# Performance work log

Hardware: AMD Instinct MI355X
Metric: run time of the kernel (lower is better)

## Reference

```python
import jax, jax.numpy as jnp
import numpy as np
import math

B, T, D = 4, 4096, 1024
N_HEAD = 16
HEAD_DIM = D // N_HEAD
BUCKET_SIZE = 64
N_HASHES = 2
N_BUCKETS = max(1, T // BUCKET_SIZE)


def rope(x):
    # x: [B, H, T, d]; faithful to the torch module (cos/sin use cat(freqs,freqs),
    # rotation interleaves even/odd pairs)
    d = x.shape[-1]
    inv_freq = 1.0 / (10000.0 ** (jnp.arange(0, d, 2, dtype=jnp.float32) / d))
    t = jnp.arange(x.shape[2], dtype=jnp.float32)
    freqs = jnp.einsum('i,j->ij', t, inv_freq)          # [T, d/2]
    emb = jnp.concatenate([freqs, freqs], axis=-1)      # [T, d]
    cos = jnp.cos(emb)[None, None, :, :]
    sin = jnp.sin(emb)[None, None, :, :]
    x1, x2 = x[..., ::2], x[..., 1::2]
    rotated = jnp.stack([-x2, x1], axis=-1).reshape(x.shape)
    return x * cos + rotated * sin


def setup_inputs() -> dict:
    key = jax.random.key(0)
    ks = jax.random.split(key, 6)
    x = jax.random.normal(ks[0], (B, T, D), dtype=jnp.float32)
    s = 1.0 / math.sqrt(D)
    W_attn = jax.random.normal(ks[1], (D, 3 * D), dtype=jnp.float32) * s
    b_attn = jnp.zeros((3 * D,), dtype=jnp.float32)
    W_proj = jax.random.normal(ks[2], (D, D), dtype=jnp.float32) * s
    b_proj = jnp.zeros((D,), dtype=jnp.float32)
    # Gaussian probe matrix (torch.manual_seed makes it a fixed constant per call)
    R = jax.random.normal(ks[3], (HEAD_DIM, N_HASHES, N_BUCKETS // 2), dtype=jnp.float32)
    return {"x": x, "W_attn": W_attn, "b_attn": b_attn,
            "W_proj": W_proj, "b_proj": b_proj, "R": R}


def reference(x, W_attn, b_attn, W_proj, b_proj, R):
    Bx, Tx, Dx = x.shape
    H, hd = N_HEAD, HEAD_DIM
    qkv = x @ W_attn + b_attn                            # [B, T, 3D]
    q, k, v = jnp.split(qkv, 3, axis=-1)

    def heads(t):
        return t.reshape(Bx, Tx, H, hd).transpose(0, 2, 1, 3)  # [B, H, T, hd]
    q, k, v = heads(q), heads(k), heads(v)
    q = rope(q)
    k = rope(k)

    qh = q.reshape(Bx * H, Tx, hd)
    kh = k.reshape(Bx * H, Tx, hd)
    vh = v.reshape(Bx * H, Tx, hd)

    # Gaussian probe hashing on queries
    proj = jnp.einsum('bnd,dhm->bnhm', qh, R)            # [BH, T, n_hashes, nb/2]
    proj = jnp.concatenate([proj, -proj], axis=-1)       # [BH, T, n_hashes, nb]
    buckets = jnp.argmax(proj, axis=-1)                  # [BH, T, n_hashes]
    b_idx = buckets[..., 0]                              # [BH, T]

    sorted_idx = jnp.argsort(b_idx, axis=-1)             # [BH, T]
    unsort_idx = jnp.argsort(sorted_idx, axis=-1)

    gidx = sorted_idx[..., None]
    q_sort = jnp.take_along_axis(qh, gidx, axis=1)
    k_sort = jnp.take_along_axis(kh, gidx, axis=1)
    v_sort = jnp.take_along_axis(vh, gidx, axis=1)

    chunk = BUCKET_SIZE * 2
    n_chunks = (Tx + chunk - 1) // chunk
    pad_len = n_chunks * chunk - Tx
    if pad_len > 0:
        pad = ((0, 0), (0, pad_len), (0, 0))
        q_sort = jnp.pad(q_sort, pad)
        k_sort = jnp.pad(k_sort, pad)
        v_sort = jnp.pad(v_sort, pad)

    qc = q_sort.reshape(Bx * H, n_chunks, chunk, hd)
    kc = k_sort.reshape(Bx * H, n_chunks, chunk, hd)
    vc = v_sort.reshape(Bx * H, n_chunks, chunk, hd)

    attn = jnp.einsum('bcid,bcjd->bcij', qc, kc) / math.sqrt(hd)
    attn = jax.nn.softmax(attn, axis=-1)
    out_local = jnp.einsum('bcij,bcjd->bcid', attn, vc)

    out_local = out_local.reshape(Bx * H, n_chunks * chunk, hd)[:, :Tx, :]
    out = jnp.take_along_axis(out_local, unsort_idx[..., None], axis=1)
    out = out.reshape(Bx, H, Tx, hd).transpose(0, 2, 1, 3).reshape(Bx, Tx, Dx)
    return out @ W_proj + b_proj
```

## Files before the change

kernel.cpp:

```cpp
#include <hip/hip_runtime.h>
#include <math.h>

#define Bz 4
#define Tz 4096
#define Dz 1024
#define Hz 16
#define HDz 64
#define BHz 64
#define Mz 16384

typedef __attribute__((ext_vector_type(8))) short short8;
typedef __attribute__((ext_vector_type(8))) __bf16 bf16x8;
typedef __attribute__((ext_vector_type(4))) float floatx4;

__device__ inline unsigned short f2bf(float f) {
    unsigned u = __float_as_uint(f);
    u = (u + 0x7fffu + ((u >> 16) & 1u)) >> 16;
    return (unsigned short)u;
}
__device__ inline float bf2f(unsigned short h) {
    return __uint_as_float(((unsigned)h) << 16);
}

__device__ __forceinline__ void g2l16(const void* g, void* l) {
    __builtin_amdgcn_global_load_lds(
        (const __attribute__((address_space(1))) unsigned int*)g,
        (__attribute__((address_space(3))) unsigned int*)l,
        16, 0, 0);
}

__global__ __launch_bounds__(256) void k_trig(float* __restrict__ tbl) {
    int t = blockIdx.x * 256 + threadIdx.x;
    float ft = (float)t;
    for (int j = 0; j < 64; ++j) {
        int kidx = (j < 32) ? j : (j - 32);
        double e = (double)(2 * kidx) / 64.0;
        float p = (float)pow(10000.0, e);
        float invf = 1.0f / p;
        float arg = ft * invf;
        tbl[t * 128 + j * 2 + 0] = cosf(arg);
        tbl[t * 128 + j * 2 + 1] = sinf(arg);
    }
}

__global__ __launch_bounds__(256) void k_cvtA(const float* __restrict__ x,
                                              unsigned short* __restrict__ xh,
                                              unsigned short* __restrict__ xl,
                                              unsigned short* __restrict__ xll)
{
    size_t i4 = (size_t)blockIdx.x * 256 + threadIdx.x;
    float4 v = *(const float4*)(x + i4 * 4);
    ushort4 h, l, l2;
    float r;
    h.x = f2bf(v.x); r = v.x - bf2f(h.x); l.x = f2bf(r); l2.x = f2bf(r - bf2f(l.x));
    h.y = f2bf(v.y); r = v.y - bf2f(h.y); l.y = f2bf(r); l2.y = f2bf(r - bf2f(l.y));
    h.z = f2bf(v.z); r = v.z - bf2f(h.z); l.z = f2bf(r); l2.z = f2bf(r - bf2f(l.z));
    h.w = f2bf(v.w); r = v.w - bf2f(h.w); l.w = f2bf(r); l2.w = f2bf(r - bf2f(l.w));
    *(ushort4*)(xh  + i4 * 4) = h;
    *(ushort4*)(xl  + i4 * 4) = l;
    *(ushort4*)(xll + i4 * 4) = l2;
}

__global__ __launch_bounds__(256) void k_cvtB(const float* __restrict__ W,
                                              unsigned short* __restrict__ wh,
                                              unsigned short* __restrict__ wl)
{
    __shared__ float tile[64][65];
    const int n0 = blockIdx.x * 64;
    const int k0 = blockIdx.y * 64;
    const int tid = threadIdx.x;
#pragma unroll
    for (int i = 0; i < 16; ++i) {
        int flat = i * 256 + tid;
        int kr = flat >> 6, nc = flat & 63;
        tile[kr][nc] = W[(size_t)(k0 + kr) * 3072 + 1024 + n0 + nc];
    }
    __syncthreads();
#pragma unroll
    for (int i = 0; i < 16; ++i) {
        int flat = i * 256 + tid;
        int nr = flat >> 6, kc = flat & 63;
        float v = tile[kc][nr];
        unsigned short h = f2bf(v);
        wh[(size_t)(n0 + nr) * 1024 + k0 + kc] = h;
        wl[(size_t)(n0 + nr) * 1024 + k0 + kc] = f2bf(v - bf2f(h));
    }
}

__global__ __launch_bounds__(256) void k_cvtBQ(const float* __restrict__ W,
                                               unsigned short* __restrict__ wh,
                                               unsigned short* __restrict__ wl,
                                               unsigned short* __restrict__ wll)
{
    __shared__ float tile[64][65];
    const int n0 = blockIdx.x * 64;
    const int k0 = blockIdx.y * 64;
    const int tid = threadIdx.x;
#pragma unroll
    for (int i = 0; i < 16; ++i) {
        int flat = i * 256 + tid;
        int kr = flat >> 6, nc = flat & 63;
        tile[kr][nc] = W[(size_t)(k0 + kr) * 3072 + n0 + nc];
    }
    __syncthreads();
#pragma unroll
    for (int i = 0; i < 16; ++i) {
        int flat = i * 256 + tid;
        int nr = flat >> 6, kc = flat & 63;
        float v = tile[kc][nr];
        unsigned short h = f2bf(v);
        float r1 = v - bf2f(h);
        unsigned short l = f2bf(r1);
        wh [(size_t)(n0 + nr) * 1024 + k0 + kc] = h;
        wl [(size_t)(n0 + nr) * 1024 + k0 + kc] = l;
        wll[(size_t)(n0 + nr) * 1024 + k0 + kc] = f2bf(r1 - bf2f(l));
    }
}

__global__ __launch_bounds__(256) void k_cvtP(const float* __restrict__ W,
                                              unsigned short* __restrict__ wh,
                                              unsigned short* __restrict__ wl)
{
    __shared__ float tile[64][65];
    const int n0 = blockIdx.x * 64;
    const int k0 = blockIdx.y * 64;
    const int tid = threadIdx.x;
#pragma unroll
    for (int i = 0; i < 16; ++i) {
        int flat = i * 256 + tid;
        int kr = flat >> 6, nc = flat & 63;
        tile[kr][nc] = W[(size_t)(k0 + kr) * 1024 + n0 + nc];
    }
    __syncthreads();
#pragma unroll
    for (int i = 0; i < 16; ++i) {
        int flat = i * 256 + tid;
        int nr = flat >> 6, kc = flat & 63;
        float v = tile[kc][nr];
        unsigned short h = f2bf(v);
        wh[(size_t)(n0 + nr) * 1024 + k0 + kc] = h;
        wl[(size_t)(n0 + nr) * 1024 + k0 + kc] = f2bf(v - bf2f(h));
    }
}

__global__ __launch_bounds__(256) void k_q6(const unsigned short* __restrict__ xh,
                                            const unsigned short* __restrict__ xl,
                                            const unsigned short* __restrict__ xll,
                                            const unsigned short* __restrict__ wh,
                                            const unsigned short* __restrict__ wl,
                                            const unsigned short* __restrict__ wll,
                                            const float* __restrict__ bias,
                                            const float* __restrict__ tbl,
                                            float* __restrict__ Qb)
{
    __shared__ unsigned short Ah[128 * 32], Al[128 * 32], A2[128 * 32];
    __shared__ unsigned short Bh[128 * 32], Bl[128 * 32], B2[128 * 32];
    const int tid = threadIdx.x;
    const int lane = tid & 63, wv = tid >> 6;
    const int hw = blockIdx.y * 8 + blockIdx.x;
    const int lg = (hw & 7) * 128 + (hw >> 3);
    const int n0 = (lg & 7) * 128;
    const int m0 = (lg >> 3) * 128;
    const int wm = (wv & 1) * 64, wn = (wv >> 1) * 64;
    const int sr = tid >> 2, sc = tid & 3;
    const int fr = lane & 15, fq = lane >> 4;

    floatx4 acc[4][4];
#pragma unroll
    for (int i = 0; i < 4; ++i)
#pragma unroll
        for (int j = 0; j < 4; ++j) acc[i][j] = (floatx4){0.f, 0.f, 0.f, 0.f};

    for (int kt = 0; kt < 1024; kt += 32) {
        __syncthreads();
#pragma unroll
        for (int s = 0; s < 2; ++s) {
            int row = s * 64 + sr;
            size_t ga = (size_t)(m0 + row) * 1024 + kt + sc * 8;
            size_t gb = (size_t)(n0 + row) * 1024 + kt + sc * 8;
            int lo = row * 32 + sc * 8;
            g2l16(xh  + ga, &Ah[lo]);
            g2l16(xl  + ga, &Al[lo]);
            g2l16(xll + ga, &A2[lo]);
            g2l16(wh  + gb, &Bh[lo]);
            g2l16(wl  + gb, &Bl[lo]);
            g2l16(wll + gb, &B2[lo]);
        }
        __syncthreads();

        bf16x8 a0[4], a1[4], a2[4];
#pragma unroll
        for (int i = 0; i < 4; ++i) {
            a0[i] = __builtin_bit_cast(bf16x8, *(const short8*)(&Ah[(wm + i * 16 + fr) * 32 + fq * 8]));
            a1[i] = __builtin_bit_cast(bf16x8, *(const short8*)(&Al[(wm + i * 16 + fr) * 32 + fq * 8]));
            a2[i] = __builtin_bit_cast(bf16x8, *(const short8*)(&A2[(wm + i * 16 + fr) * 32 + fq * 8]));
        }
#pragma unroll
        for (int j = 0; j < 4; ++j) {
            bf16x8 b0 = __builtin_bit_cast(bf16x8, *(const short8*)(&Bh[(wn + j * 16 + fr) * 32 + fq * 8]));
            bf16x8 b1 = __builtin_bit_cast(bf16x8, *(const short8*)(&Bl[(wn + j * 16 + fr) * 32 + fq * 8]));
            bf16x8 b2 = __builtin_bit_cast(bf16x8, *(const short8*)(&B2[(wn + j * 16 + fr) * 32 + fq * 8]));
#pragma unroll
            for (int i = 0; i < 4; ++i) {
                acc[i][j] = __builtin_amdgcn_mfma_f32_16x16x32_bf16(a0[i], b0, acc[i][j], 0, 0, 0);
                acc[i][j] = __builtin_amdgcn_mfma_f32_16x16x32_bf16(a0[i], b1, acc[i][j], 0, 0, 0);
                acc[i][j] = __builtin_amdgcn_mfma_f32_16x16x32_bf16(a1[i], b0, acc[i][j], 0, 0, 0);
                acc[i][j] = __builtin_amdgcn_mfma_f32_16x16x32_bf16(a1[i], b1, acc[i][j], 0, 0, 0);
                acc[i][j] = __builtin_amdgcn_mfma_f32_16x16x32_bf16(a0[i], b2, acc[i][j], 0, 0, 0);
                acc[i][j] = __builtin_amdgcn_mfma_f32_16x16x32_bf16(a2[i], b0, acc[i][j], 0, 0, 0);
            }
        }
    }

#pragma unroll
    for (int j = 0; j < 4; ++j) {
        int nn = n0 + wn + j * 16 + fr;
        float bv = bias[nn];
        int h = nn >> 6, d = nn & 63;
#pragma unroll
        for (int i = 0; i < 4; ++i) {
#pragma unroll
            for (int r = 0; r < 4; ++r) {
                int mm = m0 + wm + i * 16 + fq * 4 + r;
                int t = mm & 4095, bb = mm >> 12;
                float y = acc[i][j][r] + bv;
                float part = __shfl_xor(y, 1);
                float c = tbl[t * 128 + d * 2];
                float s = tbl[t * 128 + d * 2 + 1];
                float o = (d & 1) ? fmaf(part, s, y * c) : fmaf(-part, s, y * c);
                Qb[((size_t)(bb * 16 + h) * 4096 + t) * 64 + d] = o;
            }
        }
    }
}

__global__ __launch_bounds__(256) void k_kv(const unsigned short* __restrict__ xh,
                                            const unsigned short* __restrict__ xl,
                                            const unsigned short* __restrict__ wh,
                                            const unsigned short* __restrict__ wl,
                                            const float* __restrict__ bias,
                                            const float* __restrict__ tbl,
                                            float* __restrict__ Kb,
                                            float* __restrict__ Vb)
{
    __shared__ unsigned short Ah[128 * 32], Al[128 * 32], Bh[128 * 32], Bl[128 * 32];
    const int tid = threadIdx.x;
    const int lane = tid & 63, wv = tid >> 6;
    const int hw = blockIdx.y * 16 + blockIdx.x;
    const int lg = (hw & 7) * 256 + (hw >> 3);
    const int n0 = (lg & 15) * 128;
    const int m0 = (lg >> 4) * 128;
    const int wm = (wv & 1) * 64, wn = (wv >> 1) * 64;
    const int sr = tid >> 2, sc = tid & 3;
    const int fr = lane & 15, fq = lane >> 4;

    floatx4 acc[4][4];
#pragma unroll
    for (int i = 0; i < 4; ++i)
#pragma unroll
        for (int j = 0; j < 4; ++j) acc[i][j] = (floatx4){0.f, 0.f, 0.f, 0.f};

    for (int kt = 0; kt < 1024; kt += 32) {
        __syncthreads();
#pragma unroll
        for (int s = 0; s < 2; ++s) {
            int row = s * 64 + sr;
            size_t ga = (size_t)(m0 + row) * 1024 + kt + sc * 8;
            size_t gb = (size_t)(n0 + row) * 1024 + kt + sc * 8;
            int lo = row * 32 + sc * 8;
            g2l16(xh + ga, &Ah[lo]);
            g2l16(xl + ga, &Al[lo]);
            g2l16(wh + gb, &Bh[lo]);
            g2l16(wl + gb, &Bl[lo]);
        }
        __syncthreads();

        bf16x8 afh[4], afl[4], bfh[4], bfl[4];
#pragma unroll
        for (int i = 0; i < 4; ++i) {
            afh[i] = __builtin_bit_cast(bf16x8, *(const short8*)(&Ah[(wm + i * 16 + fr) * 32 + fq * 8]));
            afl[i] = __builtin_bit_cast(bf16x8, *(const short8*)(&Al[(wm + i * 16 + fr) * 32 + fq * 8]));
            bfh[i] = __builtin_bit_cast(bf16x8, *(const short8*)(&Bh[(wn + i * 16 + fr) * 32 + fq * 8]));
            bfl[i] = __builtin_bit_cast(bf16x8, *(const short8*)(&Bl[(wn + i * 16 + fr) * 32 + fq * 8]));
        }
#pragma unroll
        for (int i = 0; i < 4; ++i)
#pragma unroll
            for (int j = 0; j < 4; ++j) {
                acc[i][j] = __builtin_amdgcn_mfma_f32_16x16x32_bf16(afh[i], bfh[j], acc[i][j], 0, 0, 0);
                acc[i][j] = __builtin_amdgcn_mfma_f32_16x16x32_bf16(afh[i], bfl[j], acc[i][j], 0, 0, 0);
                acc[i][j] = __builtin_amdgcn_mfma_f32_16x16x32_bf16(afl[i], bfh[j], acc[i][j], 0, 0, 0);
            }
    }

#pragma unroll
    for (int j = 0; j < 4; ++j) {
        int nn = n0 + wn + j * 16 + fr;
        float bv = bias[1024 + nn];
#pragma unroll
        for (int i = 0; i < 4; ++i) {
#pragma unroll
            for (int r = 0; r < 4; ++r) {
                int mm = m0 + wm + i * 16 + fq * 4 + r;
                int t = mm & 4095, bb = mm >> 12;
                float y = acc[i][j][r] + bv;
                if (nn < 1024) {
                    int h = nn >> 6, d = nn & 63;
                    float part = __shfl_xor(y, 1);
                    float c = tbl[t * 128 + d * 2];
                    float s = tbl[t * 128 + d * 2 + 1];
                    float o = (d & 1) ? fmaf(part, s, y * c) : fmaf(-part, s, y * c);
                    Kb[((size_t)(bb * 16 + h) * 4096 + t) * 64 + d] = o;
                } else {
                    int nv = nn - 1024;
                    int h = nv >> 6, d = nv & 63;
                    Vb[((size_t)(bb * 16 + h) * 4096 + t) * 64 + d] = y;
                }
            }
        }
    }
}

__global__ __launch_bounds__(64) void k_bucket(const float* __restrict__ Q,
                                               const float* __restrict__ R,
                                               int* __restrict__ bidx)
{
    __shared__ float Qs[64][65];
    __shared__ float Rs[64][32];
    const int tid = threadIdx.x;
    const int g0 = blockIdx.x * 64;
    const int bh = g0 >> 12;
    const int t0 = g0 & 4095;
#pragma unroll
    for (int m = 0; m < 32; ++m) Rs[tid][m] = R[tid * 64 + m];
    const float* qbase = Q + ((size_t)bh * Tz + t0) * 64;
    for (int r = 0; r < 64; ++r) Qs[r][tid] = qbase[(size_t)r * 64 + tid];
    __syncthreads();

    float s[32];
#pragma unroll
    for (int m = 0; m < 32; ++m) s[m] = 0.f;
    for (int d = 0; d < 64; ++d) {
        float qd = Qs[tid][d];
#pragma unroll
        for (int m4 = 0; m4 < 8; ++m4) {
            float4 r4 = *(const float4*)(&Rs[d][m4 * 4]);
            s[m4 * 4 + 0] = fmaf(qd, r4.x, s[m4 * 4 + 0]);
            s[m4 * 4 + 1] = fmaf(qd, r4.y, s[m4 * 4 + 1]);
            s[m4 * 4 + 2] = fmaf(qd, r4.z, s[m4 * 4 + 2]);
            s[m4 * 4 + 3] = fmaf(qd, r4.w, s[m4 * 4 + 3]);
        }
    }
    float best = s[0];
    int bi = 0;
#pragma unroll
    for (int m = 1; m < 64; ++m) {
        float v = (m < 32) ? s[m] : -s[m - 32];
        if (v > best) { best = v; bi = m; }
    }
    bidx[g0 + tid] = bi;
}

__global__ __launch_bounds__(64) void k_sort(const int* __restrict__ bidx,
                                             int* __restrict__ sidx)
{
    __shared__ int lb[4096];
    __shared__ int ls[4096];
    __shared__ int runTot[64];
    __shared__ int base[64];
    const int lane = threadIdx.x;
    const int bh = blockIdx.x;
    const int* brow = bidx + (size_t)bh * 4096;
    for (int i = lane; i < 4096; i += 64) lb[i] = brow[i];
    runTot[lane] = 0;

    const unsigned long long lmask = (1ull << lane) - 1ull;
    for (int r = 0; r < 64; ++r) {
        int i = r * 64 + lane;
        int k = lb[i];
        unsigned long long m = ~0ull;
#pragma unroll
        for (int b = 0; b < 6; ++b) {
            unsigned long long bb = __ballot((k >> b) & 1);
            m &= ((k >> b) & 1) ? bb : ~bb;
        }
        int rank = __popcll(m & lmask);
        int before = runTot[k];
        lb[i] = (k << 16) | (before + rank);
        if (rank == 0) runTot[k] = before + __popcll(m);
    }
    int tot = runTot[lane];
    int run = tot;
#pragma unroll
    for (int off = 1; off < 64; off <<= 1) {
        int n = __shfl_up(run, off, 64);
        if (lane >= off) run += n;
    }
    base[lane] = run - tot;
    for (int r = 0; r < 64; ++r) {
        int i = r * 64 + lane;
        int v = lb[i];
        ls[base[v >> 16] + (v & 0xffff)] = i;
    }
    int* srow = sidx + (size_t)bh * 4096;
    for (int i = lane; i < 4096; i += 64) srow[i] = ls[i];
}

__global__ __launch_bounds__(256) void k_attn(const float* __restrict__ Q,
                                              const float* __restrict__ Kg,
                                              const float* __restrict__ Vg,
                                              const int* __restrict__ sidx,
                                              unsigned short* __restrict__ AOh,
                                              unsigned short* __restrict__ AOl)
{
    __shared__ unsigned short smem[27648];
    unsigned short* KhS = smem;
    unsigned short* KlS = smem + 9216;
    unsigned short* PbS = smem;
    unsigned short* VtS = smem + 18432;

    const int hw = blockIdx.y * 32 + blockIdx.x;
    const int lg = (hw & 7) * 256 + (hw >> 3);
    const int ch = lg & 31;
    const int bh = lg >> 5;
    const int tid = threadIdx.x;
    const int lane = tid & 63;
    const int w = tid >> 6;
    const int c = lane & 15;
    const int q = lane >> 4;
    const int* srow = sidx + (size_t)bh * Tz + ch * 128;

    {
        const int r = tid >> 1;
        const int d0 = (tid & 1) * 32;
        int orig = srow[r];
        const float* kp = Kg + ((size_t)bh * Tz + orig) * 64 + d0;
        const float* vp = Vg + ((size_t)bh * Tz + orig) * 64 + d0;
#pragma unroll
        for (int j4 = 0; j4 < 8; ++j4) {
            float4 k4 = *(const float4*)(kp + j4 * 4);
            ushort4 h4, l4;
            h4.x = f2bf(k4.x); l4.x = f2bf(k4.x - bf2f(h4.x));
            h4.y = f2bf(k4.y); l4.y = f2bf(k4.y - bf2f(h4.y));
            h4.z = f2bf(k4.z); l4.z = f2bf(k4.z - bf2f(h4.z));
            h4.w = f2bf(k4.w); l4.w = f2bf(k4.w - bf2f(h4.w));
            *(ushort4*)(&KhS[r * 72 + d0 + j4 * 4]) = h4;
            *(ushort4*)(&KlS[r * 72 + d0 + j4 * 4]) = l4;
            float4 v4 = *(const float4*)(vp + j4 * 4);
            int db = d0 + j4 * 4;
            VtS[(db + 0) * 144 + r] = f2bf(v4.x);
            VtS[(db + 1) * 144 + r] = f2bf(v4.y);
            VtS[(db + 2) * 144 + r] = f2bf(v4.z);
            VtS[(db + 3) * 144 + r] = f2bf(v4.w);
        }
    }

    bf16x8 qh[2][2], ql[2][2];
#pragma unroll
    for (int i = 0; i < 2; ++i) {
        int row = w * 32 + i * 16 + c;
        int orig = srow[row];
        const float* qp = Q + ((size_t)bh * Tz + orig) * 64 + q * 8;
#pragma unroll
        for (int kc = 0; kc < 2; ++kc) {
            float4 fa = *(const float4*)(qp + kc * 32);
            float4 fb = *(const float4*)(qp + kc * 32 + 4);
            float f[8] = {fa.x, fa.y, fa.z, fa.w, fb.x, fb.y, fb.z, fb.w};
            short8 hh, ll;
#pragma unroll
            for (int e = 0; e < 8; ++e) {
                unsigned short h = f2bf(f[e]);
                hh[e] = (short)h;
                ll[e] = (short)f2bf(f[e] - bf2f(h));
            }
            qh[i][kc] = __builtin_bit_cast(bf16x8, hh);
            ql[i][kc] = __builtin_bit_cast(bf16x8, ll);
        }
    }
    __syncthreads();

    floatx4 accs[2][8];
#pragma unroll
    for (int i = 0; i < 2; ++i)
#pragma unroll
        for (int j = 0; j < 8; ++j) accs[i][j] = (floatx4){0.f, 0.f, 0.f, 0.f};

#pragma unroll
    for (int j = 0; j < 8; ++j) {
        int n = j * 16 + c;
        bf16x8 kbh[2], kbl[2];
#pragma unroll
        for (int kc = 0; kc < 2; ++kc) {
            kbh[kc] = __builtin_bit_cast(bf16x8, *(const short8*)(&KhS[n * 72 + kc * 32 + q * 8]));
            kbl[kc] = __builtin_bit_cast(bf16x8, *(const short8*)(&KlS[n * 72 + kc * 32 + q * 8]));
        }
#pragma unroll
        for (int i = 0; i < 2; ++i)
#pragma unroll
            for (int kc = 0; kc < 2; ++kc) {
                accs[i][j] = __builtin_amdgcn_mfma_f32_16x16x32_bf16(qh[i][kc], kbh[kc], accs[i][j], 0, 0, 0);
                accs[i][j] = __builtin_amdgcn_mfma_f32_16x16x32_bf16(qh[i][kc], kbl[kc], accs[i][j], 0, 0, 0);
                accs[i][j] = __builtin_amdgcn_mfma_f32_16x16x32_bf16(ql[i][kc], kbh[kc], accs[i][j], 0, 0, 0);
            }
    }

    float linv[2][4];
#pragma unroll
    for (int i = 0; i < 2; ++i) {
#pragma unroll
        for (int r = 0; r < 4; ++r) {
            float mm = -1e30f;
#pragma unroll
            for (int j = 0; j < 8; ++j) {
                float v = accs[i][j][r] * 0.125f;
                accs[i][j][r] = v;
                mm = fmaxf(mm, v);
            }
#pragma unroll
            for (int off = 1; off < 16; off <<= 1) mm = fmaxf(mm, __shfl_xor(mm, off));
            float ss = 0.f;
#pragma unroll
            for (int j = 0; j < 8; ++j) {
                float p = expf(accs[i][j][r] - mm);
                accs[i][j][r] = p;
                ss += p;
            }
#pragma unroll
            for (int off = 1; off < 16; off <<= 1) ss += __shfl_xor(ss, off);
            linv[i][r] = 1.0f / ss;
        }
    }
    __syncthreads();

#pragma unroll
    for (int i = 0; i < 2; ++i)
#pragma unroll
        for (int j = 0; j < 8; ++j)
#pragma unroll
            for (int r = 0; r < 4; ++r)
                PbS[(w * 32 + i * 16 + q * 4 + r) * 144 + j * 16 + c] = f2bf(accs[i][j][r]);

    floatx4 acco[2][4];
#pragma unroll
    for (int i = 0; i < 2; ++i)
#pragma unroll
        for (int jf = 0; jf < 4; ++jf) acco[i][jf] = (floatx4){0.f, 0.f, 0.f, 0.f};

#pragma unroll
    for (int kc = 0; kc < 4; ++kc) {
        bf16x8 pa[2];
#pragma unroll
        for (int i = 0; i < 2; ++i)
            pa[i] = __builtin_bit_cast(bf16x8, *(const short8*)(&PbS[(w * 32 + i * 16 + c) * 144 + kc * 32 + q * 8]));
#pragma unroll
        for (int jf = 0; jf < 4; ++jf) {
            bf16x8 vb = __builtin_bit_cast(bf16x8, *(const short8*)(&VtS[(jf * 16 + c) * 144 + kc * 32 + q * 8]));
            acco[0][jf] = __builtin_amdgcn_mfma_f32_16x16x32_bf16(pa[0], vb, acco[0][jf], 0, 0, 0);
            acco[1][jf] = __builtin_amdgcn_mfma_f32_16x16x32_bf16(pa[1], vb, acco[1][jf], 0, 0, 0);
        }
    }

    const int bb = bh >> 4, hh = bh & 15;
#pragma unroll
    for (int i = 0; i < 2; ++i) {
#pragma unroll
        for (int r = 0; r < 4; ++r) {
            int row = w * 32 + i * 16 + q * 4 + r;
            int orig = srow[row];
            float inv = linv[i][r];
            size_t base = ((size_t)bb * 4096 + orig) * 1024 + hh * 64 + c;
#pragma unroll
            for (int jf = 0; jf < 4; ++jf) {
                float val = acco[i][jf][r] * inv;
                unsigned short h = f2bf(val);
                unsigned short l = f2bf(val - bf2f(h));
                AOh[base + jf * 16] = h;
                AOl[base + jf * 16] = l;
            }
        }
    }
}

__global__ __launch_bounds__(256) void k_proj(const unsigned short* __restrict__ ah,
                                              const unsigned short* __restrict__ al,
                                              const unsigned short* __restrict__ wh,
                                              const unsigned short* __restrict__ wl,
                                              const float* __restrict__ bias,
                                              float* __restrict__ Cout)
{
    __shared__ unsigned short Ah[128 * 32], Al[128 * 32], Bh[128 * 32], Bl[128 * 32];
    const int tid = threadIdx.x;
    const int lane = tid & 63, wv = tid >> 6;
    const int hw = blockIdx.y * 8 + blockIdx.x;
    const int lg = (hw & 7) * 128 + (hw >> 3);
    const int n0 = (lg & 7) * 128;
    const int m0 = (lg >> 3) * 128;
    const int wm = (wv & 1) * 64, wn = (wv >> 1) * 64;
    const int sr = tid >> 2, sc = tid & 3;
    const int fr = lane & 15, fq = lane >> 4;

    floatx4 acc[4][4];
#pragma unroll
    for (int i = 0; i < 4; ++i)
#pragma unroll
        for (int j = 0; j < 4; ++j) acc[i][j] = (floatx4){0.f, 0.f, 0.f, 0.f};

    for (int kt = 0; kt < 1024; kt += 32) {
        __syncthreads();
#pragma unroll
        for (int s = 0; s < 2; ++s) {
            int row = s * 64 + sr;
            size_t ga = (size_t)(m0 + row) * 1024 + kt + sc * 8;
            size_t gb = (size_t)(n0 + row) * 1024 + kt + sc * 8;
            int lo = row * 32 + sc * 8;
            g2l16(ah + ga, &Ah[lo]);
            g2l16(al + ga, &Al[lo]);
            g2l16(wh + gb, &Bh[lo]);
            g2l16(wl + gb, &Bl[lo]);
        }
        __syncthreads();

        bf16x8 afh[4], afl[4], bfh[4], bfl[4];
#pragma unroll
        for (int i = 0; i < 4; ++i) {
            afh[i] = __builtin_bit_cast(bf16x8, *(const short8*)(&Ah[(wm + i * 16 + fr) * 32 + fq * 8]));
            afl[i] = __builtin_bit_cast(bf16x8, *(const short8*)(&Al[(wm + i * 16 + fr) * 32 + fq * 8]));
            bfh[i] = __builtin_bit_cast(bf16x8, *(const short8*)(&Bh[(wn + i * 16 + fr) * 32 + fq * 8]));
            bfl[i] = __builtin_bit_cast(bf16x8, *(const short8*)(&Bl[(wn + i * 16 + fr) * 32 + fq * 8]));
        }
#pragma unroll
        for (int i = 0; i < 4; ++i)
#pragma unroll
            for (int j = 0; j < 4; ++j) {
                acc[i][j] = __builtin_amdgcn_mfma_f32_16x16x32_bf16(afh[i], bfh[j], acc[i][j], 0, 0, 0);
                acc[i][j] = __builtin_amdgcn_mfma_f32_16x16x32_bf16(afh[i], bfl[j], acc[i][j], 0, 0, 0);
                acc[i][j] = __builtin_amdgcn_mfma_f32_16x16x32_bf16(afl[i], bfh[j], acc[i][j], 0, 0, 0);
            }
    }

#pragma unroll
    for (int j = 0; j < 4; ++j) {
        int nn = n0 + wn + j * 16 + fr;
        float bv = bias[nn];
#pragma unroll
        for (int i = 0; i < 4; ++i) {
#pragma unroll
            for (int r = 0; r < 4; ++r) {
                int mm = m0 + wm + i * 16 + fq * 4 + r;
                Cout[(size_t)mm * 1024 + nn] = acc[i][j][r] + bv;
            }
        }
    }
}

extern "C" void kernel_launch(void* const* d_in, const int* in_sizes, int n_in,
                              void* d_out, int out_size, void* d_ws, size_t ws_size,
                              hipStream_t stream)
{
    const float* x      = (const float*)d_in[0];
    const float* W_attn = (const float*)d_in[1];
    const float* b_attn = (const float*)d_in[2];
    const float* W_proj = (const float*)d_in[3];
    const float* b_proj = (const float*)d_in[4];
    const float* R      = (const float*)d_in[5];
    float* out = (float*)d_out;

    char* ws = (char*)d_ws;
    const size_t MB = 1024 * 1024;
    float*          tbl  = (float*)(ws);
    float*          Qb   = (float*)(ws + 2 * MB);
    float*          Kb   = (float*)(ws + 66 * MB);
    unsigned short* xll  = (unsigned short*)(ws + 66 * MB);
    unsigned short* wqh  = (unsigned short*)(ws + 98 * MB);
    unsigned short* wql  = (unsigned short*)(ws + 100 * MB);
    unsigned short* wqll = (unsigned short*)(ws + 102 * MB);
    unsigned short* xh   = (unsigned short*)(ws + 130 * MB);
    unsigned short* xl   = (unsigned short*)(ws + 162 * MB);
    unsigned short* AOh  = (unsigned short*)(ws + 130 * MB);
    unsigned short* AOl  = (unsigned short*)(ws + 162 * MB);
    int*            bidx = (int*)(ws + 194 * MB);
    int*            sidx = (int*)(ws + 195 * MB);
    unsigned short* wth  = (unsigned short*)(ws + 196 * MB);
    unsigned short* wtl  = (unsigned short*)(ws + 200 * MB);
    unsigned short* wph  = (unsigned short*)(ws + 196 * MB);
    unsigned short* wpl  = (unsigned short*)(ws + 200 * MB);
    float*          Vb   = (float*)d_out;

    k_trig  <<<dim3(16),       dim3(256), 0, stream>>>(tbl);
    k_cvtA  <<<dim3(16384),    dim3(256), 0, stream>>>(x, xh, xl, xll);
    k_cvtB  <<<dim3(32, 16),   dim3(256), 0, stream>>>(W_attn, wth, wtl);
    k_cvtBQ <<<dim3(16, 16),   dim3(256), 0, stream>>>(W_attn, wqh, wql, wqll);
    k_q6    <<<dim3(8, 128),   dim3(256), 0, stream>>>(xh, xl, xll, wqh, wql, wqll, b_attn, tbl, Qb);
    k_kv    <<<dim3(16, 128),  dim3(256), 0, stream>>>(xh, xl, wth, wtl, b_attn, tbl, Kb, Vb);
    k_cvtP  <<<dim3(16, 16),   dim3(256), 0, stream>>>(W_proj, wph, wpl);
    k_bucket<<<dim3(4096),     dim3(64),  0, stream>>>(Qb, R, bidx);
    k_sort  <<<dim3(64),       dim3(64),  0, stream>>>(bidx, sidx);
    k_attn  <<<dim3(32, 64),   dim3(256), 0, stream>>>(Qb, Kb, Vb, sidx, AOh, AOl);
    k_proj  <<<dim3(8, 128),   dim3(256), 0, stream>>>(AOh, AOl, wph, wpl, b_proj, out);
}
```

Before: 824.3 us.

## Use 256x128 tiles with 512-thread blocks in GEMMs, split Q GEMM into two passes, parallelize trig table

The three split-bf16 GEMM kernels (Q, KV, proj) move from 128x128 tiles with 256 threads to 256x128 tiles with 512 threads. This raises reuse of each staged B tile and halves B traffic per output. The Q kernel now runs two K passes with only two LDS planes instead of six, trading extra A/B staging traffic for lower LDS footprint and register pressure. The trig table kernel assigns one thread per (t, j) pair instead of looping over 64 j values, so it launches far more blocks. Risks are lower occupancy from the larger blocks and the extra global reloads in the Q pass split.

Result: slower. 962.6 us (+16.8%).

```diff
diff --git a/kernel.cpp b/kernel.cpp
--- a/kernel.cpp
+++ b/kernel.cpp
@@ -30,17 +30,16 @@
 }
 
 __global__ __launch_bounds__(256) void k_trig(float* __restrict__ tbl) {
-    int t = blockIdx.x * 256 + threadIdx.x;
-    float ft = (float)t;
-    for (int j = 0; j < 64; ++j) {
-        int kidx = (j < 32) ? j : (j - 32);
-        double e = (double)(2 * kidx) / 64.0;
-        float p = (float)pow(10000.0, e);
-        float invf = 1.0f / p;
-        float arg = ft * invf;
-        tbl[t * 128 + j * 2 + 0] = cosf(arg);
-        tbl[t * 128 + j * 2 + 1] = sinf(arg);
-    }
+    int gid = blockIdx.x * 256 + threadIdx.x;
+    int t = gid >> 6;
+    int j = gid & 63;
+    int kidx = (j < 32) ? j : (j - 32);
+    double e = (double)(2 * kidx) / 64.0;
+    float p = (float)pow(10000.0, e);
+    float invf = 1.0f / p;
+    float arg = (float)t * invf;
+    tbl[t * 128 + j * 2 + 0] = cosf(arg);
+    tbl[t * 128 + j * 2 + 1] = sinf(arg);
 }
 
 __global__ __launch_bounds__(256) void k_cvtA(const float* __restrict__ x,
@@ -143,7 +142,7 @@
     }
 }
 
-__global__ __launch_bounds__(256) void k_q6(const unsigned short* __restrict__ xh,
+__global__ __launch_bounds__(512) void k_q6(const unsigned short* __restrict__ xh,
                                             const unsigned short* __restrict__ xl,
                                             const unsigned short* __restrict__ xll,
                                             const unsigned short* __restrict__ wh,
@@ -153,16 +152,16 @@
                                             const float* __restrict__ tbl,
                                             float* __restrict__ Qb)
 {
-    __shared__ unsigned short Ah[128 * 32], Al[128 * 32], A2[128 * 32];
-    __shared__ unsigned short Bh[128 * 32], Bl[128 * 32], B2[128 * 32];
+    __shared__ unsigned short A0s[256 * 32], A1s[256 * 32];
+    __shared__ unsigned short B0s[128 * 32], B1s[128 * 32];
     const int tid = threadIdx.x;
     const int lane = tid & 63, wv = tid >> 6;
     const int hw = blockIdx.y * 8 + blockIdx.x;
-    const int lg = (hw & 7) * 128 + (hw >> 3);
+    const int lg = (hw & 7) * 64 + (hw >> 3);
     const int n0 = (lg & 7) * 128;
-    const int m0 = (lg >> 3) * 128;
-    const int wm = (wv & 1) * 64, wn = (wv >> 1) * 64;
-    const int sr = tid >> 2, sc = tid & 3;
+    const int m0 = (lg >> 3) * 256;
+    const int wm = (wv & 3) * 64, wn = (wv >> 2) * 64;
+    const int sra = tid >> 2, sca = tid & 3;
     const int fr = lane & 15, fq = lane >> 4;
 
     floatx4 acc[4][4];
@@ -171,43 +170,52 @@
 #pragma unroll
         for (int j = 0; j < 4; ++j) acc[i][j] = (floatx4){0.f, 0.f, 0.f, 0.f};
 
-    for (int kt = 0; kt < 1024; kt += 32) {
-        __syncthreads();
+    auto stage = [&](const unsigned short* a1, const unsigned short* b1, int kt) {
 #pragma unroll
         for (int s = 0; s < 2; ++s) {
-            int row = s * 64 + sr;
-            size_t ga = (size_t)(m0 + row) * 1024 + kt + sc * 8;
-            size_t gb = (size_t)(n0 + row) * 1024 + kt + sc * 8;
-            int lo = row * 32 + sc * 8;
-            g2l16(xh  + ga, &Ah[lo]);
-            g2l16(xl  + ga, &Al[lo]);
-            g2l16(xll + ga, &A2[lo]);
-            g2l16(wh  + gb, &Bh[lo]);
-            g2l16(wl  + gb, &Bl[lo]);
-            g2l16(wll + gb, &B2[lo]);
-        }
-        __syncthreads();
-
-        bf16x8 a0[4], a1[4], a2[4];
-#pragma unroll
-        for (int i = 0; i < 4; ++i) {
-            a0[i] = __builtin_bit_cast(bf16x8, *(const short8*)(&Ah[(wm + i * 16 + fr) * 32 + fq * 8]));
-            a1[i] = __builtin_bit_cast(bf16x8, *(const short8*)(&Al[(wm + i * 16 + fr) * 32 + fq * 8]));
-            a2[i] = __builtin_bit_cast(bf16x8, *(const short8*)(&A2[(wm + i * 16 + fr) * 32 + fq * 8]));
-        }
-#pragma unroll
-        for (int j = 0; j < 4; ++j) {
-            bf16x8 b0 = __builtin_bit_cast(bf16x8, *(const short8*)(&Bh[(wn + j * 16 + fr) * 32 + fq * 8]));
-            bf16x8 b1 = __builtin_bit_cast(bf16x8, *(const short8*)(&Bl[(wn + j * 16 + fr) * 32 + fq * 8]));
-            bf16x8 b2 = __builtin_bit_cast(bf16x8, *(const short8*)(&B2[(wn + j * 16 + fr) * 32 + fq * 8]));
+            int row = s * 128 + sra;
+            size_t ga = (size_t)(m0 + row) * 1024 + kt + sca * 8;
+            int lo = row * 32 + sca * 8;
+            g2l16(xh + ga, &A0s[lo]);
+            g2l16(a1 + ga, &A1s[lo]);
+        }
+        int rb = sra;
+        size_t gb = (size_t)(n0 + rb) * 1024 + kt + sca * 8;
+        int lb_ = rb * 32 + sca * 8;
+        g2l16(wh + gb, &B0s[lb_]);
+        g2l16(b1 + gb, &B1s[lb_]);
+    };
+
+    for (int pass = 0; pass < 2; ++pass) {
+        const unsigned short* a1 = pass ? xll : xl;
+        const unsigned short* b1 = pass ? wll : wl;
+        for (int kt = 0; kt < 1024; kt += 32) {
+            __syncthreads();
+            stage(a1, b1, kt);
+            __syncthreads();
+
+            bf16x8 a0[4], a1f[4];
 #pragma unroll
             for (int i = 0; i < 4; ++i) {
-                acc[i][j] = __builtin_amdgcn_mfma_f32_16x16x32_bf16(a0[i], b0, acc[i][j], 0, 0, 0);
-                acc[i][j] = __builtin_amdgcn_mfma_f32_16x16x32_bf16(a0[i], b1, acc[i][j], 0, 0, 0);
-                acc[i][j] = __builtin_amdgcn_mfma_f32_16x16x32_bf16(a1[i], b0, acc[i][j], 0, 0, 0);
-                acc[i][j] = __builtin_amdgcn_mfma_f32_16x16x32_bf16(a1[i], b1, acc[i][j], 0, 0, 0);
-                acc[i][j] = __builtin_amdgcn_mfma_f32_16x16x32_bf16(a0[i], b2, acc[i][j], 0, 0, 0);
-                acc[i][j] = __builtin_amdgcn_mfma_f32_16x16x32_bf16(a2[i], b0, acc[i][j], 0, 0, 0);
+                a0[i]  = __builtin_bit_cast(bf16x8, *(const short8*)(&A0s[(wm + i * 16 + fr) * 32 + fq * 8]));
+                a1f[i] = __builtin_bit_cast(bf16x8, *(const short8*)(&A1s[(wm + i * 16 + fr) * 32 + fq * 8]));
+            }
+#pragma unroll
+            for (int j = 0; j < 4; ++j) {
+                bf16x8 b0 = __builtin_bit_cast(bf16x8, *(const short8*)(&B0s[(wn + j * 16 + fr) * 32 + fq * 8]));
+                bf16x8 b1f = __builtin_bit_cast(bf16x8, *(const short8*)(&B1s[(wn + j * 16 + fr) * 32 + fq * 8]));
+#pragma unroll
+                for (int i = 0; i < 4; ++i) {
+                    if (pass == 0) {
+                        acc[i][j] = __builtin_amdgcn_mfma_f32_16x16x32_bf16(a0[i],  b0,  acc[i][j], 0, 0, 0);
+                        acc[i][j] = __builtin_amdgcn_mfma_f32_16x16x32_bf16(a0[i],  b1f, acc[i][j], 0, 0, 0);
+                        acc[i][j] = __builtin_amdgcn_mfma_f32_16x16x32_bf16(a1f[i], b0,  acc[i][j], 0, 0, 0);
+                        acc[i][j] = __builtin_amdgcn_mfma_f32_16x16x32_bf16(a1f[i], b1f, acc[i][j], 0, 0, 0);
+                    } else {
+                        acc[i][j] = __builtin_amdgcn_mfma_f32_16x16x32_bf16(a0[i],  b1f, acc[i][j], 0, 0, 0);
+                        acc[i][j] = __builtin_amdgcn_mfma_f32_16x16x32_bf16(a1f[i], b0,  acc[i][j], 0, 0, 0);
+                    }
+                }
             }
         }
     }
@@ -234,7 +242,7 @@
     }
 }
 
-__global__ __launch_bounds__(256) void k_kv(const unsigned short* __restrict__ xh,
+__global__ __launch_bounds__(512) void k_kv(const unsigned short* __restrict__ xh,
                                             const unsigned short* __restrict__ xl,
                                             const unsigned short* __restrict__ wh,
                                             const unsigned short* __restrict__ wl,
@@ -243,15 +251,16 @@
                                             float* __restrict__ Kb,
                                             float* __restrict__ Vb)
 {
-    __shared__ unsigned short Ah[128 * 32], Al[128 * 32], Bh[128 * 32], Bl[128 * 32];
+    __shared__ unsigned short Ah[256 * 32], Al[256 * 32];
+    __shared__ unsigned short Bh[128 * 32], Bl[128 * 32];
     const int tid = threadIdx.x;
     const int lane = tid & 63, wv = tid >> 6;
-    const int hw = blockIdx.y * 16 + blockIdx.x;
-    const int lg = (hw & 7) * 256 + (hw >> 3);
+    const int hw = blockIdx.y * 8 + blockIdx.x;
+    const int lg = (hw & 7) * 128 + (hw >> 3);
     const int n0 = (lg & 15) * 128;
-    const int m0 = (lg >> 4) * 128;
-    const int wm = (wv & 1) * 64, wn = (wv >> 1) * 64;
-    const int sr = tid >> 2, sc = tid & 3;
+    const int m0 = (lg >> 4) * 256;
+    const int wm = (wv & 3) * 64, wn = (wv >> 2) * 64;
+    const int sra = tid >> 2, sca = tid & 3;
     const int fr = lane & 15, fq = lane >> 4;
 
     floatx4 acc[4][4];
@@ -264,33 +273,38 @@
         __syncthreads();
 #pragma unroll
         for (int s = 0; s < 2; ++s) {
-            int row = s * 64 + sr;
-            size_t ga = (size_t)(m0 + row) * 1024 + kt + sc * 8;
-            size_t gb = (size_t)(n0 + row) * 1024 + kt + sc * 8;
-            int lo = row * 32 + sc * 8;
+            int row = s * 128 + sra;
+            size_t ga = (size_t)(m0 + row) * 1024 + kt + sca * 8;
+            int lo = row * 32 + sca * 8;
             g2l16(xh + ga, &Ah[lo]);
             g2l16(xl + ga, &Al[lo]);
-            g2l16(wh + gb, &Bh[lo]);
-            g2l16(wl + gb, &Bl[lo]);
+        }
+        {
+            int rb = sra;
+            size_t gb = (size_t)(n0 + rb) * 1024 + kt + sca * 8;
+            int lb_ = rb * 32 + sca * 8;
+            g2l16(wh + gb, &Bh[lb_]);
+            g2l16(wl + gb, &Bl[lb_]);
         }
         __syncthreads();
 
-        bf16x8 afh[4], afl[4], bfh[4], bfl[4];
+        bf16x8 afh[4], afl[4];
 #pragma unroll
         for (int i = 0; i < 4; ++i) {
             afh[i] = __builtin_bit_cast(bf16x8, *(const short8*)(&Ah[(wm + i * 16 + fr) * 32 + fq * 8]));
             afl[i] = __builtin_bit_cast(bf16x8, *(const short8*)(&Al[(wm + i * 16 + fr) * 32 + fq * 8]));
-            bfh[i] = __builtin_bit_cast(bf16x8, *(const short8*)(&Bh[(wn + i * 16 + fr) * 32 + fq * 8]));
-            bfl[i] = __builtin_bit_cast(bf16x8, *(const short8*)(&Bl[(wn + i * 16 + fr) * 32 + fq * 8]));
-        }
-#pragma unroll
-        for (int i = 0; i < 4; ++i)
-#pragma unroll
-            for (int j = 0; j < 4; ++j) {
-                acc[i][j] = __builtin_amdgcn_mfma_f32_16x16x32_bf16(afh[i], bfh[j], acc[i][j], 0, 0, 0);
-                acc[i][j] = __builtin_amdgcn_mfma_f32_16x16x32_bf16(afh[i], bfl[j], acc[i][j], 0, 0, 0);
-                acc[i][j] = __builtin_amdgcn_mfma_f32_16x16x32_bf16(afl[i], bfh[j], acc[i][j], 0, 0, 0);
-            }
+        }
+#pragma unroll
+        for (int j = 0; j < 4; ++j) {
+            bf16x8 bfh = __builtin_bit_cast(bf16x8, *(const short8*)(&Bh[(wn + j * 16 + fr) * 32 + fq * 8]));
+            bf16x8 bfl = __builtin_bit_cast(bf16x8, *(const short8*)(&Bl[(wn + j * 16 + fr) * 32 + fq * 8]));
+#pragma unroll
+            for (int i = 0; i < 4; ++i) {
+                acc[i][j] = __builtin_amdgcn_mfma_f32_16x16x32_bf16(afh[i], bfh, acc[i][j], 0, 0, 0);
+                acc[i][j] = __builtin_amdgcn_mfma_f32_16x16x32_bf16(afh[i], bfl, acc[i][j], 0, 0, 0);
+                acc[i][j] = __builtin_amdgcn_mfma_f32_16x16x32_bf16(afl[i], bfh, acc[i][j], 0, 0, 0);
+            }
+        }
     }
 
 #pragma unroll
@@ -581,22 +595,23 @@
     }
 }
 
-__global__ __launch_bounds__(256) void k_proj(const unsigned short* __restrict__ ah,
+__global__ __launch_bounds__(512) void k_proj(const unsigned short* __restrict__ ah,
                                               const unsigned short* __restrict__ al,
                                               const unsigned short* __restrict__ wh,
                                               const unsigned short* __restrict__ wl,
                                               const float* __restrict__ bias,
                                               float* __restrict__ Cout)
 {
-    __shared__ unsigned short Ah[128 * 32], Al[128 * 32], Bh[128 * 32], Bl[128 * 32];
+    __shared__ unsigned short Ah[256 * 32], Al[256 * 32];
+    __shared__ unsigned short Bh[128 * 32], Bl[128 * 32];
     const int tid = threadIdx.x;
     const int lane = tid & 63, wv = tid >> 6;
     const int hw = blockIdx.y * 8 + blockIdx.x;
-    const int lg = (hw & 7) * 128 + (hw >> 3);
+    const int lg = (hw & 7) * 64 + (hw >> 3);
     const int n0 = (lg & 7) * 128;
-    const int m0 = (lg >> 3) * 128;
-    const int wm = (wv & 1) * 64, wn = (wv >> 1) * 64;
-    const int sr = tid >> 2, sc = tid & 3;
+    const int m0 = (lg >> 3) * 256;
+    const int wm = (wv & 3) * 64, wn = (wv >> 2) * 64;
+    const int sra = tid >> 2, sca = tid & 3;
     const int fr = lane & 15, fq = lane >> 4;
 
     floatx4 acc[4][4];
@@ -609,33 +624,38 @@
         __syncthreads();
 #pragma unroll
         for (int s = 0; s < 2; ++s) {
-            int row = s * 64 + sr;
-            size_t ga = (size_t)(m0 + row) * 1024 + kt + sc * 8;
-            size_t gb = (size_t)(n0 + row) * 1024 + kt + sc * 8;
-            int lo = row * 32 + sc * 8;
+            int row = s * 128 + sra;
+            size_t ga = (size_t)(m0 + row) * 1024 + kt + sca * 8;
+            int lo = row * 32 + sca * 8;
             g2l16(ah + ga, &Ah[lo]);
             g2l16(al + ga, &Al[lo]);
-            g2l16(wh + gb, &Bh[lo]);
-            g2l16(wl + gb, &Bl[lo]);
+        }
+        {
+            int rb = sra;
+            size_t gb = (size_t)(n0 + rb) * 1024 + kt + sca * 8;
+            int lb_ = rb * 32 + sca * 8;
+            g2l16(wh + gb, &Bh[lb_]);
+            g2l16(wl + gb, &Bl[lb_]);
         }
         __syncthreads();
 
-        bf16x8 afh[4], afl[4], bfh[4], bfl[4];
+        bf16x8 afh[4], afl[4];
 #pragma unroll
         for (int i = 0; i < 4; ++i) {
             afh[i] = __builtin_bit_cast(bf16x8, *(const short8*)(&Ah[(wm + i * 16 + fr) * 32 + fq * 8]));
             afl[i] = __builtin_bit_cast(bf16x8, *(const short8*)(&Al[(wm + i * 16 + fr) * 32 + fq * 8]));
-            bfh[i] = __builtin_bit_cast(bf16x8, *(const short8*)(&Bh[(wn + i * 16 + fr) * 32 + fq * 8]));
-            bfl[i] = __builtin_bit_cast(bf16x8, *(const short8*)(&Bl[(wn + i * 16 + fr) * 32 + fq * 8]));
-        }
-#pragma unroll
-        for (int i = 0; i < 4; ++i)
-#pragma unroll
-            for (int j = 0; j < 4; ++j) {
-                acc[i][j] = __builtin_amdgcn_mfma_f32_16x16x32_bf16(afh[i], bfh[j], acc[i][j], 0, 0, 0);
-                acc[i][j] = __builtin_amdgcn_mfma_f32_16x16x32_bf16(afh[i], bfl[j], acc[i][j], 0, 0, 0);
-                acc[i][j] = __builtin_amdgcn_mfma_f32_16x16x32_bf16(afl[i], bfh[j], acc[i][j], 0, 0, 0);
-            }
+        }
+#pragma unroll
+        for (int j = 0; j < 4; ++j) {
+            bf16x8 bfh = __builtin_bit_cast(bf16x8, *(const short8*)(&Bh[(wn + j * 16 + fr) * 32 + fq * 8]));
+            bf16x8 bfl = __builtin_bit_cast(bf16x8, *(const short8*)(&Bl[(wn + j * 16 + fr) * 32 + fq * 8]));
+#pragma unroll
+            for (int i = 0; i < 4; ++i) {
+                acc[i][j] = __builtin_amdgcn_mfma_f32_16x16x32_bf16(afh[i], bfh, acc[i][j], 0, 0, 0);
+                acc[i][j] = __builtin_amdgcn_mfma_f32_16x16x32_bf16(afh[i], bfl, acc[i][j], 0, 0, 0);
+                acc[i][j] = __builtin_amdgcn_mfma_f32_16x16x32_bf16(afl[i], bfh, acc[i][j], 0, 0, 0);
+            }
+        }
     }
 
 #pragma unroll
@@ -686,15 +706,15 @@
     unsigned short* wpl  = (unsigned short*)(ws + 200 * MB);
     float*          Vb   = (float*)d_out;
 
-    k_trig  <<<dim3(16),       dim3(256), 0, stream>>>(tbl);
+    k_trig  <<<dim3(1024),     dim3(256), 0, stream>>>(tbl);
     k_cvtA  <<<dim3(16384),    dim3(256), 0, stream>>>(x, xh, xl, xll);
     k_cvtB  <<<dim3(32, 16),   dim3(256), 0, stream>>>(W_attn, wth, wtl);
     k_cvtBQ <<<dim3(16, 16),   dim3(256), 0, stream>>>(W_attn, wqh, wql, wqll);
-    k_q6    <<<dim3(8, 128),   dim3(256), 0, stream>>>(xh, xl, xll, wqh, wql, wqll, b_attn, tbl, Qb);
-    k_kv    <<<dim3(16, 128),  dim3(256), 0, stream>>>(xh, xl, wth, wtl, b_attn, tbl, Kb, Vb);
+    k_q6    <<<dim3(8, 64),    dim3(512), 0, stream>>>(xh, xl, xll, wqh, wql, wqll, b_attn, tbl, Qb);
+    k_kv    <<<dim3(8, 128),   dim3(512), 0, stream>>>(xh, xl, wth, wtl, b_attn, tbl, Kb, Vb);
     k_cvtP  <<<dim3(16, 16),   dim3(256), 0, stream>>>(W_proj, wph, wpl);
     k_bucket<<<dim3(4096),     dim3(64),  0, stream>>>(Qb, R, bidx);
     k_sort  <<<dim3(64),       dim3(64),  0, stream>>>(bidx, sidx);
     k_attn  <<<dim3(32, 64),   dim3(256), 0, stream>>>(Qb, Kb, Vb, sidx, AOh, AOl);
-    k_proj  <<<dim3(8, 128),   dim3(256), 0, stream>>>(AOh, AOl, wph, wpl, b_proj, out);
-}
+    k_proj  <<<dim3(8, 64),    dim3(512), 0, stream>>>(AOh, AOl, wph, wpl, b_proj, out);
+}
```
